# Performance work log

Hardware: AMD Instinct MI355X
Metric: run time of the kernel (lower is better)

The kernel has to match this reference:

```python
import jax, jax.numpy as jnp
import numpy as np

N = 10000      # nodes
E = 160000     # directed edges (avg degree 16)
F_IN = 2208    # num_features (DenseNet-161 dim)
H = 512        # hidden_channels
C = 2          # num_classes


def setup_inputs() -> dict:
    key = jax.random.key(0)
    ks = jax.random.split(key, 10)
    x = jax.random.normal(ks[0], (N, F_IN), dtype=jnp.float32)
    edge_index = jax.random.randint(ks[1], (2, E), 0, N, dtype=jnp.int64)
    batch = jnp.zeros((N,), dtype=jnp.int64)

    def glorot(k, fan_in, fan_out):
        s = np.sqrt(6.0 / (fan_in + fan_out)).astype(np.float32)
        return jax.random.uniform(k, (fan_in, fan_out), jnp.float32, -s, s)

    return {
        "x": x,
        "edge_index": edge_index,
        "batch": batch,
        "W1": glorot(ks[2], F_IN, H), "b1": jnp.zeros((H,), jnp.float32),
        "W2": glorot(ks[3], H, H),    "b2": jnp.zeros((H,), jnp.float32),
        "W3": glorot(ks[4], H, H),    "b3": jnp.zeros((H,), jnp.float32),
        "W4": glorot(ks[5], H, C),    "b4": jnp.zeros((C,), jnp.float32),
    }


def reference(x, edge_index, batch, W1, b1, W2, b2, W3, b3, W4, b4):
    # GCNConv (PyG defaults): add self-loops, symmetric normalization
    # out = D^{-1/2} (A + I) D^{-1/2} X W + b. Norm depends only on the
    # graph, so compute it once and reuse across the 4 layers.
    src, dst = edge_index[0], edge_index[1]
    loop = jnp.arange(N, dtype=edge_index.dtype)
    s = jnp.concatenate([src, loop])  # [E+N]
    d = jnp.concatenate([dst, loop])  # [E+N]
    deg = jax.ops.segment_sum(jnp.ones(E + N, x.dtype), d, num_segments=N)
    dinv = jnp.where(deg > 0, jax.lax.rsqrt(deg), 0.0)
    norm = dinv[s] * dinv[d]          # [E+N] per-edge weight

    def conv(h, W, b):
        h = h @ W                                 # [N, out] dense GEMM first (PyG order)
        msg = h[s] * norm[:, None]                # gather + scale  [E+N, out]
        return jax.ops.segment_sum(msg, d, num_segments=N) + b

    h = jax.nn.relu(conv(x, W1, b1))   # dropout p=0.3 is identity in eval mode
    h = jax.nn.relu(conv(h, W2, b2))
    h = jax.nn.relu(conv(h, W3, b3))
    h = conv(h, W4, b4)
    return jax.nn.log_softmax(h, axis=1)
```

## Files before the change

### kernel.cpp

```cpp
#include <hip/hip_runtime.h>
#include <hip/hip_bf16.h>

#define NNODES 10000
#define NEDGES 160000
#define FIN    2208
#define HDIM   512
#define NCLS   2

#define MPAD   10240
#define K1PAD  2240
#define BCAP   128

typedef __bf16 bf16x8 __attribute__((ext_vector_type(8)));
typedef float  f32x4  __attribute__((ext_vector_type(4)));
typedef unsigned short u16x8 __attribute__((ext_vector_type(8)));

__device__ inline unsigned short f2bf(float f) {
    union { float f; unsigned int u; } v; v.f = f;
    return (unsigned short)((v.u + 0x7FFFu + ((v.u >> 16) & 1u)) >> 16);
}
__device__ inline float bf2f(unsigned short u) {
    union { unsigned int i; float f; } v; v.i = ((unsigned int)u) << 16; return v.f;
}

__global__ void k_prep(const float* __restrict__ W1, const float* __restrict__ W2,
                       const float* __restrict__ W3, unsigned short* __restrict__ W1t,
                       unsigned short* __restrict__ W2t, unsigned short* __restrict__ W3t,
                       int* __restrict__ cnt) {
    int n = blockIdx.y;
    int bx = blockIdx.x;
    int t = threadIdx.x;
    if (bx < 9) {
        int k = bx * 256 + t;
        if (k < K1PAD) {
            float v = (k < FIN) ? W1[(size_t)k * HDIM + n] : 0.0f;
            W1t[(size_t)n * K1PAD + k] = f2bf(v);
        }
    } else if (bx < 11) {
        int k = (bx - 9) * 256 + t;
        W2t[(size_t)n * HDIM + k] = f2bf(W2[(size_t)k * HDIM + n]);
    } else if (bx < 13) {
        int k = (bx - 11) * 256 + t;
        W3t[(size_t)n * HDIM + k] = f2bf(W3[(size_t)k * HDIM + n]);
    } else {
        int i = n * 256 + t;
        if (i < NNODES) cnt[i] = 0;
    }
}

__global__ void k_cvt_fill(const float* __restrict__ x, unsigned short* __restrict__ xb,
                           const int* __restrict__ ei, int* __restrict__ cnt,
                           int* __restrict__ bucket) {
    int bx = blockIdx.x;
    int t = threadIdx.x;
    if (bx >= MPAD) {
        int i = (bx - MPAD) * 256 + t;
        if (i < NEDGES) {
            int src = ei[i];
            int dst = ei[NEDGES + i];
            int pos = atomicAdd(&cnt[dst], 1);
            bucket[dst * BCAP + pos] = src;
        }
        return;
    }
    int row = bx;
    unsigned short* orow = xb + (size_t)row * K1PAD;
    u16x8 z = {0, 0, 0, 0, 0, 0, 0, 0};
    if (row >= NNODES) {
        for (int c = t; c < K1PAD / 8; c += 256) *(u16x8*)(orow + c * 8) = z;
        return;
    }
    const float* irow = x + (size_t)row * FIN;
    for (int c = t; c < K1PAD / 8; c += 256) {
        int col = c * 8;
        u16x8 o = z;
        if (col + 8 <= FIN) {
            float4 f0 = *(const float4*)(irow + col);
            float4 f1 = *(const float4*)(irow + col + 4);
            o[0] = f2bf(f0.x); o[1] = f2bf(f0.y); o[2] = f2bf(f0.z); o[3] = f2bf(f0.w);
            o[4] = f2bf(f1.x); o[5] = f2bf(f1.y); o[6] = f2bf(f1.z); o[7] = f2bf(f1.w);
        }
        *(u16x8*)(orow + col) = o;
    }
}

#define BKK 64
#define GG1 640

__device__ __forceinline__ void gemm_body(
    const unsigned short* __restrict__ A, const unsigned short* __restrict__ Bt,
    unsigned short* __restrict__ C, int M, int K, int l) {
    __shared__ char As[128 * BKK * 2] __attribute__((aligned(16)));
    __shared__ char Bs[64 * BKK * 2]  __attribute__((aligned(16)));
    const int tid  = threadIdx.x;
    const int lane = tid & 63;
    const int w    = tid >> 6;
    const int wm   = w & 1, wn = w >> 1;
    const int quad = lane >> 4, lq = lane & 15;

    const int xcd   = l & 7;
    const int q     = l >> 3;
    const int strip = (q >> 3) * 8 + xcd;
    const int bm    = strip * 128;
    const int bn    = (q & 7) * 64;

    f32x4 acc[4][2] = {};

    for (int k0 = 0; k0 < K; k0 += BKK) {
        #pragma unroll
        for (int i = 0; i < 4; ++i) {
            int c = i * 256 + tid;
            int r = c >> 3;
            int g = (c & 7) ^ (r & 7);
            const char* gpA = (const char*)A + ((size_t)(bm + r) * K + k0) * 2 + (g << 4);
            __builtin_amdgcn_global_load_lds(
                (const __attribute__((address_space(1))) void*)gpA,
                (__attribute__((address_space(3))) void*)(As + c * 16), 16, 0, 0);
        }
        #pragma unroll
        for (int i = 0; i < 2; ++i) {
            int c = i * 256 + tid;
            int r = c >> 3;
            int g = (c & 7) ^ (r & 7);
            const char* gpB = (const char*)Bt + ((size_t)(bn + r) * K + k0) * 2 + (g << 4);
            __builtin_amdgcn_global_load_lds(
                (const __attribute__((address_space(1))) void*)gpB,
                (__attribute__((address_space(3))) void*)(Bs + c * 16), 16, 0, 0);
        }
        __syncthreads();

        #pragma unroll
        for (int s = 0; s < 2; ++s) {
            bf16x8 af[4], bfr[2];
            int g = s * 4 + quad;
            #pragma unroll
            for (int i = 0; i < 4; ++i) {
                int r = wm * 64 + i * 16 + lq;
                af[i] = *(const bf16x8*)(As + r * 128 + ((g ^ (r & 7)) << 4));
            }
            #pragma unroll
            for (int j = 0; j < 2; ++j) {
                int n = wn * 32 + j * 16 + lq;
                bfr[j] = *(const bf16x8*)(Bs + n * 128 + ((g ^ (n & 7)) << 4));
            }
            #pragma unroll
            for (int i = 0; i < 4; ++i)
                #pragma unroll
                for (int j = 0; j < 2; ++j)
                    acc[i][j] = __builtin_amdgcn_mfma_f32_16x16x32_bf16(
                        af[i], bfr[j], acc[i][j], 0, 0, 0);
        }
        __syncthreads();
    }

    #pragma unroll
    for (int i = 0; i < 4; ++i) {
        #pragma unroll
        for (int p = 0; p < 4; ++p) {
            int r = bm + wm * 64 + i * 16 + quad * 4 + p;
            if (r < M) {
                #pragma unroll
                for (int j = 0; j < 2; ++j) {
                    int col = bn + wn * 32 + j * 16 + lq;
                    C[(size_t)r * HDIM + col] = f2bf(acc[i][j][p]);
                }
            }
        }
    }
}

__global__ __launch_bounds__(256) void k_gemm1_dinv(
    const unsigned short* __restrict__ A, const unsigned short* __restrict__ Bt,
    unsigned short* __restrict__ C, int M, int K,
    const int* __restrict__ cnt, float* __restrict__ dinv) {
    int bx = blockIdx.x;
    if (bx < GG1) { gemm_body(A, Bt, C, M, K, bx); return; }
    int i = (bx - GG1) * 256 + threadIdx.x;
    if (i < NNODES) dinv[i] = rsqrtf((float)cnt[i] + 1.0f);
}

__global__ __launch_bounds__(256) void k_gemm_bf16(
    const unsigned short* __restrict__ A, const unsigned short* __restrict__ Bt,
    unsigned short* __restrict__ C, int M, int K) {
    gemm_body(A, Bt, C, M, K, blockIdx.x);
}


__global__ void k_agg(const unsigned short* __restrict__ Y, const float* __restrict__ dinv,
                      const int* __restrict__ cnt, const int* __restrict__ bucket,
                      const float* __restrict__ bias, unsigned short* __restrict__ Hb) {
    int w = (blockIdx.x * blockDim.x + threadIdx.x) >> 6;
    int lane = threadIdx.x & 63;
    if (w >= MPAD) return;
    unsigned short* hr = Hb + (size_t)w * HDIM + lane * 8;
    if (w >= NNODES) {
        u16x8 z = {0, 0, 0, 0, 0, 0, 0, 0};
        *(u16x8*)hr = z;
        return;
    }
    float di = dinv[w];
    float sw = di * di;
    u16x8 own = *(const u16x8*)(Y + (size_t)w * HDIM + lane * 8);
    float acc[8];
    #pragma unroll
    for (int t = 0; t < 8; ++t) acc[t] = sw * bf2f(own[t]);

    const int* col = bucket + w * BCAP;
    int deg = cnt[w];
    int e = 0;
    for (; e + 4 <= deg; e += 4) {
        int s0 = col[e + 0], s1 = col[e + 1];
        int s2 = col[e + 2], s3 = col[e + 3];
        float w0 = di * dinv[s0], w1 = di * dinv[s1];
        float w2 = di * dinv[s2], w3 = di * dinv[s3];
        u16x8 v0 = *(const u16x8*)(Y + (size_t)s0 * HDIM + lane * 8);
        u16x8 v1 = *(const u16x8*)(Y + (size_t)s1 * HDIM + lane * 8);
        u16x8 v2 = *(const u16x8*)(Y + (size_t)s2 * HDIM + lane * 8);
        u16x8 v3 = *(const u16x8*)(Y + (size_t)s3 * HDIM + lane * 8);
        #pragma unroll
        for (int t = 0; t < 8; ++t) {
            acc[t] += w0 * bf2f(v0[t]);
            acc[t] += w1 * bf2f(v1[t]);
            acc[t] += w2 * bf2f(v2[t]);
            acc[t] += w3 * bf2f(v3[t]);
        }
    }
    for (; e < deg; ++e) {
        int s = col[e];
        float wg = di * dinv[s];
        u16x8 v = *(const u16x8*)(Y + (size_t)s * HDIM + lane * 8);
        #pragma unroll
        for (int t = 0; t < 8; ++t) acc[t] += wg * bf2f(v[t]);
    }

    float4 b0 = ((const float4*)bias)[lane * 2];
    float4 b1 = ((const float4*)bias)[lane * 2 + 1];
    acc[0] += b0.x; acc[1] += b0.y; acc[2] += b0.z; acc[3] += b0.w;
    acc[4] += b1.x; acc[5] += b1.y; acc[6] += b1.z; acc[7] += b1.w;
    u16x8 o;
    #pragma unroll
    for (int t = 0; t < 8; ++t) o[t] = f2bf(fmaxf(acc[t], 0.0f));
    *(u16x8*)hr = o;
}


__global__ void k_agg_g4(const unsigned short* __restrict__ Y, const float* __restrict__ dinv,
                         const int* __restrict__ cnt, const int* __restrict__ bucket,
                         const float* __restrict__ b3, const float* __restrict__ W4,
                         float* __restrict__ Y4) {
    int w = (blockIdx.x * blockDim.x + threadIdx.x) >> 6;
    int lane = threadIdx.x & 63;
    if (w >= NNODES) return;
    float di = dinv[w];
    float sw = di * di;
    u16x8 own = *(const u16x8*)(Y + (size_t)w * HDIM + lane * 8);
    float acc[8];
    #pragma unroll
    for (int t = 0; t < 8; ++t) acc[t] = sw * bf2f(own[t]);

    const int* col = bucket + w * BCAP;
    int deg = cnt[w];
    int e = 0;
    for (; e + 4 <= deg; e += 4) {
        int s0 = col[e + 0], s1 = col[e + 1];
        int s2 = col[e + 2], s3 = col[e + 3];
        float w0 = di * dinv[s0], w1 = di * dinv[s1];
        float w2 = di * dinv[s2], w3 = di * dinv[s3];
        u16x8 v0 = *(const u16x8*)(Y + (size_t)s0 * HDIM + lane * 8);
        u16x8 v1 = *(const u16x8*)(Y + (size_t)s1 * HDIM + lane * 8);
        u16x8 v2 = *(const u16x8*)(Y + (size_t)s2 * HDIM + lane * 8);
        u16x8 v3 = *(const u16x8*)(Y + (size_t)s3 * HDIM + lane * 8);
        #pragma unroll
        for (int t = 0; t < 8; ++t) {
            acc[t] += w0 * bf2f(v0[t]);
            acc[t] += w1 * bf2f(v1[t]);
            acc[t] += w2 * bf2f(v2[t]);
            acc[t] += w3 * bf2f(v3[t]);
        }
    }
    for (; e < deg; ++e) {
        int s = col[e];
        float wg = di * dinv[s];
        u16x8 v = *(const u16x8*)(Y + (size_t)s * HDIM + lane * 8);
        #pragma unroll
        for (int t = 0; t < 8; ++t) acc[t] += wg * bf2f(v[t]);
    }

    float4 b0 = ((const float4*)b3)[lane * 2];
    float4 b1 = ((const float4*)b3)[lane * 2 + 1];
    acc[0] += b0.x; acc[1] += b0.y; acc[2] += b0.z; acc[3] += b0.w;
    acc[4] += b1.x; acc[5] += b1.y; acc[6] += b1.z; acc[7] += b1.w;
    #pragma unroll
    for (int t = 0; t < 8; ++t) acc[t] = fmaxf(acc[t], 0.0f);

    const float4* wf = (const float4*)W4;
    float4 w0 = wf[lane * 4 + 0];
    float4 w1 = wf[lane * 4 + 1];
    float4 w2 = wf[lane * 4 + 2];
    float4 w3 = wf[lane * 4 + 3];
    float z0 = acc[0]*w0.x + acc[1]*w0.z + acc[2]*w1.x + acc[3]*w1.z
             + acc[4]*w2.x + acc[5]*w2.z + acc[6]*w3.x + acc[7]*w3.z;
    float z1 = acc[0]*w0.y + acc[1]*w0.w + acc[2]*w1.y + acc[3]*w1.w
             + acc[4]*w2.y + acc[5]*w2.w + acc[6]*w3.y + acc[7]*w3.w;
    #pragma unroll
    for (int off = 32; off > 0; off >>= 1) {
        z0 += __shfl_down(z0, off);
        z1 += __shfl_down(z1, off);
    }
    if (lane == 0) {
        Y4[2 * w] = z0;
        Y4[2 * w + 1] = z1;
    }
}


__global__ void k_final(const float* __restrict__ Y4, const float* __restrict__ dinv,
                        const int* __restrict__ cnt, const int* __restrict__ bucket,
                        const float* __restrict__ b4, float* __restrict__ out, int n) {
    int i = blockIdx.x * blockDim.x + threadIdx.x;
    if (i >= n) return;
    float di = dinv[i];
    float sw = di * di;
    float z0 = sw * Y4[2 * i];
    float z1 = sw * Y4[2 * i + 1];
    const int* col = bucket + i * BCAP;
    int deg = cnt[i];
    for (int e = 0; e < deg; ++e) {
        int s = col[e];
        float wgt = di * dinv[s];
        z0 += wgt * Y4[2 * s];
        z1 += wgt * Y4[2 * s + 1];
    }
    z0 += b4[0];
    z1 += b4[1];
    float m = fmaxf(z0, z1);
    float l = m + logf(expf(z0 - m) + expf(z1 - m));
    out[2 * i] = z0 - l;
    out[2 * i + 1] = z1 - l;
}


extern "C" void kernel_launch(void* const* d_in, const int* in_sizes, int n_in,
                              void* d_out, int out_size, void* d_ws, size_t ws_size,
                              hipStream_t stream) {
    const float* x  = (const float*)d_in[0];
    const int*   ei = (const int*)d_in[1];
    const float* W1 = (const float*)d_in[3];
    const float* b1 = (const float*)d_in[4];
    const float* W2 = (const float*)d_in[5];
    const float* b2 = (const float*)d_in[6];
    const float* W3 = (const float*)d_in[7];
    const float* b3 = (const float*)d_in[8];
    const float* W4 = (const float*)d_in[9];
    const float* b4 = (const float*)d_in[10];
    float* out = (float*)d_out;

    char* ws = (char*)d_ws;
    float*          dinv    = (float*)(ws + 0);
    int*            cnt     = (int*)  (ws + 40960);
    int*            bucket  = (int*)  (ws + 81920);
    float*          Y4      = (float*)(ws + 5201920);
    unsigned short* xb      = (unsigned short*)(ws + 5283840);
    unsigned short* W1t     = (unsigned short*)(ws + 51159040);
    unsigned short* W2t     = (unsigned short*)(ws + 53452800);
    unsigned short* W3t     = (unsigned short*)(ws + 53977088);
    unsigned short* Yb      = (unsigned short*)(ws + 54501376);
    unsigned short* Hb      = (unsigned short*)(ws + 64987136);
    if (ws_size < 75472896) return;

    const int agrid = (MPAD * 64) / 256;

    k_prep<<<dim3(14, HDIM), 256, 0, stream>>>(W1, W2, W3, W1t, W2t, W3t, cnt);
    k_cvt_fill<<<MPAD + 625, 256, 0, stream>>>(x, xb, ei, cnt, bucket);
    k_gemm1_dinv<<<GG1 + 40, 256, 0, stream>>>(xb, W1t, Yb, NNODES, K1PAD, cnt, dinv);
    k_agg<<<agrid, 256, 0, stream>>>(Yb, dinv, cnt, bucket, b1, Hb);
    k_gemm_bf16<<<GG1, 256, 0, stream>>>(Hb, W2t, Yb, NNODES, HDIM);
    k_agg<<<agrid, 256, 0, stream>>>(Yb, dinv, cnt, bucket, b2, Hb);
    k_gemm_bf16<<<GG1, 256, 0, stream>>>(Hb, W3t, Yb, NNODES, HDIM);
    k_agg_g4<<<(NNODES * 64) / 256, 256, 0, stream>>>(Yb, dinv, cnt, bucket, b3, W4, Y4);
    k_final<<<40, 256, 0, stream>>>(Y4, dinv, cnt, bucket, b4, out, NNODES);
}
```

Before: 310.5 us.

## Enlarge GEMM tile to 128x128 and fuse weight prep with x conversion

The GEMM block tile grows from 128x64 to 128x128, so each wave computes a 64x64 sub-tile with 16 accumulators and the grid drops from 640 to 320 blocks. This raises reuse of the A tile and halves A reloads from global memory. Separately, weight transpose, x conversion and edge bucketing are merged into one launch, with a small zeroing kernel placed before it. The trade-offs are higher register and LDS use per block and fewer blocks (320) spread over the CUs, which could hurt occupancy.

Result: slower. 323.8 us (+4.3%).

```diff
diff --git a/kernel.cpp b/kernel.cpp
--- a/kernel.cpp
+++ b/kernel.cpp
@@ -23,75 +23,78 @@
     union { unsigned int i; float f; } v; v.i = ((unsigned int)u) << 16; return v.f;
 }
 
-__global__ void k_prep(const float* __restrict__ W1, const float* __restrict__ W2,
-                       const float* __restrict__ W3, unsigned short* __restrict__ W1t,
-                       unsigned short* __restrict__ W2t, unsigned short* __restrict__ W3t,
-                       int* __restrict__ cnt) {
-    int n = blockIdx.y;
-    int bx = blockIdx.x;
+__global__ void k_zero(int* __restrict__ cnt) {
+    int i = blockIdx.x * 256 + threadIdx.x;
+    if (i < NNODES) cnt[i] = 0;
+}
+
+#define PREPB 7168
+#define CVTB  10240
+__global__ void k_prep_cvt_fill(
+    const float* __restrict__ W1, const float* __restrict__ W2,
+    const float* __restrict__ W3, unsigned short* __restrict__ W1t,
+    unsigned short* __restrict__ W2t, unsigned short* __restrict__ W3t,
+    const float* __restrict__ x, unsigned short* __restrict__ xb,
+    const int* __restrict__ ei, int* __restrict__ cnt, int* __restrict__ bucket) {
+    int b = blockIdx.x;
     int t = threadIdx.x;
-    if (bx < 9) {
-        int k = bx * 256 + t;
-        if (k < K1PAD) {
-            float v = (k < FIN) ? W1[(size_t)k * HDIM + n] : 0.0f;
-            W1t[(size_t)n * K1PAD + k] = f2bf(v);
-        }
-    } else if (bx < 11) {
-        int k = (bx - 9) * 256 + t;
-        W2t[(size_t)n * HDIM + k] = f2bf(W2[(size_t)k * HDIM + n]);
-    } else if (bx < 13) {
-        int k = (bx - 11) * 256 + t;
-        W3t[(size_t)n * HDIM + k] = f2bf(W3[(size_t)k * HDIM + n]);
-    } else {
-        int i = n * 256 + t;
-        if (i < NNODES) cnt[i] = 0;
-    }
-}
-
-__global__ void k_cvt_fill(const float* __restrict__ x, unsigned short* __restrict__ xb,
-                           const int* __restrict__ ei, int* __restrict__ cnt,
-                           int* __restrict__ bucket) {
-    int bx = blockIdx.x;
-    int t = threadIdx.x;
-    if (bx >= MPAD) {
-        int i = (bx - MPAD) * 256 + t;
-        if (i < NEDGES) {
-            int src = ei[i];
-            int dst = ei[NEDGES + i];
-            int pos = atomicAdd(&cnt[dst], 1);
-            bucket[dst * BCAP + pos] = src;
+    if (b < PREPB) {
+        int bx = b % 14;
+        int n  = b / 14;
+        if (bx < 9) {
+            int k = bx * 256 + t;
+            if (k < K1PAD) {
+                float v = (k < FIN) ? W1[(size_t)k * HDIM + n] : 0.0f;
+                W1t[(size_t)n * K1PAD + k] = f2bf(v);
+            }
+        } else if (bx < 11) {
+            int k = (bx - 9) * 256 + t;
+            W2t[(size_t)n * HDIM + k] = f2bf(W2[(size_t)k * HDIM + n]);
+        } else if (bx < 13) {
+            int k = (bx - 11) * 256 + t;
+            W3t[(size_t)n * HDIM + k] = f2bf(W3[(size_t)k * HDIM + n]);
         }
         return;
     }
-    int row = bx;
-    unsigned short* orow = xb + (size_t)row * K1PAD;
-    u16x8 z = {0, 0, 0, 0, 0, 0, 0, 0};
-    if (row >= NNODES) {
-        for (int c = t; c < K1PAD / 8; c += 256) *(u16x8*)(orow + c * 8) = z;
+    if (b < PREPB + CVTB) {
+        int row = b - PREPB;
+        unsigned short* orow = xb + (size_t)row * K1PAD;
+        u16x8 z = {0, 0, 0, 0, 0, 0, 0, 0};
+        if (row >= NNODES) {
+            for (int c = t; c < K1PAD / 8; c += 256) *(u16x8*)(orow + c * 8) = z;
+            return;
+        }
+        const float* irow = x + (size_t)row * FIN;
+        for (int c = t; c < K1PAD / 8; c += 256) {
+            int col = c * 8;
+            u16x8 o = z;
+            if (col + 8 <= FIN) {
+                float4 f0 = *(const float4*)(irow + col);
+                float4 f1 = *(const float4*)(irow + col + 4);
+                o[0] = f2bf(f0.x); o[1] = f2bf(f0.y); o[2] = f2bf(f0.z); o[3] = f2bf(f0.w);
+                o[4] = f2bf(f1.x); o[5] = f2bf(f1.y); o[6] = f2bf(f1.z); o[7] = f2bf(f1.w);
+            }
+            *(u16x8*)(orow + col) = o;
+        }
         return;
     }
-    const float* irow = x + (size_t)row * FIN;
-    for (int c = t; c < K1PAD / 8; c += 256) {
-        int col = c * 8;
-        u16x8 o = z;
-        if (col + 8 <= FIN) {
-            float4 f0 = *(const float4*)(irow + col);
-            float4 f1 = *(const float4*)(irow + col + 4);
-            o[0] = f2bf(f0.x); o[1] = f2bf(f0.y); o[2] = f2bf(f0.z); o[3] = f2bf(f0.w);
-            o[4] = f2bf(f1.x); o[5] = f2bf(f1.y); o[6] = f2bf(f1.z); o[7] = f2bf(f1.w);
-        }
-        *(u16x8*)(orow + col) = o;
+    int i = (b - PREPB - CVTB) * 256 + t;
+    if (i < NEDGES) {
+        int src = ei[i];
+        int dst = ei[NEDGES + i];
+        int pos = atomicAdd(&cnt[dst], 1);
+        bucket[dst * BCAP + pos] = src;
     }
 }
 
 #define BKK 64
-#define GG1 640
+#define GB1 320
 
 __device__ __forceinline__ void gemm_body(
     const unsigned short* __restrict__ A, const unsigned short* __restrict__ Bt,
     unsigned short* __restrict__ C, int M, int K, int l) {
     __shared__ char As[128 * BKK * 2] __attribute__((aligned(16)));
-    __shared__ char Bs[64 * BKK * 2]  __attribute__((aligned(16)));
+    __shared__ char Bs[128 * BKK * 2] __attribute__((aligned(16)));
     const int tid  = threadIdx.x;
     const int lane = tid & 63;
     const int w    = tid >> 6;
@@ -100,11 +103,11 @@
 
     const int xcd   = l & 7;
     const int q     = l >> 3;
-    const int strip = (q >> 3) * 8 + xcd;
+    const int bn    = (q & 3) * 128;
+    const int strip = (q >> 2) * 8 + xcd;
     const int bm    = strip * 128;
-    const int bn    = (q & 7) * 64;
-
-    f32x4 acc[4][2] = {};
+
+    f32x4 acc[4][4] = {};
 
     for (int k0 = 0; k0 < K; k0 += BKK) {
         #pragma unroll
@@ -118,7 +121,7 @@
                 (__attribute__((address_space(3))) void*)(As + c * 16), 16, 0, 0);
         }
         #pragma unroll
-        for (int i = 0; i < 2; ++i) {
+        for (int i = 0; i < 4; ++i) {
             int c = i * 256 + tid;
             int r = c >> 3;
             int g = (c & 7) ^ (r & 7);
@@ -131,7 +134,7 @@
 
         #pragma unroll
         for (int s = 0; s < 2; ++s) {
-            bf16x8 af[4], bfr[2];
+            bf16x8 af[4], bfr[4];
             int g = s * 4 + quad;
             #pragma unroll
             for (int i = 0; i < 4; ++i) {
@@ -139,14 +142,14 @@
                 af[i] = *(const bf16x8*)(As + r * 128 + ((g ^ (r & 7)) << 4));
             }
             #pragma unroll
-            for (int j = 0; j < 2; ++j) {
-                int n = wn * 32 + j * 16 + lq;
+            for (int j = 0; j < 4; ++j) {
+                int n = wn * 64 + j * 16 + lq;
                 bfr[j] = *(const bf16x8*)(Bs + n * 128 + ((g ^ (n & 7)) << 4));
             }
             #pragma unroll
             for (int i = 0; i < 4; ++i)
                 #pragma unroll
-                for (int j = 0; j < 2; ++j)
+                for (int j = 0; j < 4; ++j)
                     acc[i][j] = __builtin_amdgcn_mfma_f32_16x16x32_bf16(
                         af[i], bfr[j], acc[i][j], 0, 0, 0);
         }
@@ -160,8 +163,8 @@
             int r = bm + wm * 64 + i * 16 + quad * 4 + p;
             if (r < M) {
                 #pragma unroll
-                for (int j = 0; j < 2; ++j) {
-                    int col = bn + wn * 32 + j * 16 + lq;
+                for (int j = 0; j < 4; ++j) {
+                    int col = bn + wn * 64 + j * 16 + lq;
                     C[(size_t)r * HDIM + col] = f2bf(acc[i][j][p]);
                 }
             }
@@ -174,8 +177,8 @@
     unsigned short* __restrict__ C, int M, int K,
     const int* __restrict__ cnt, float* __restrict__ dinv) {
     int bx = blockIdx.x;
-    if (bx < GG1) { gemm_body(A, Bt, C, M, K, bx); return; }
-    int i = (bx - GG1) * 256 + threadIdx.x;
+    if (bx < GB1) { gemm_body(A, Bt, C, M, K, bx); return; }
+    int i = (bx - GB1) * 256 + threadIdx.x;
     if (i < NNODES) dinv[i] = rsqrtf((float)cnt[i] + 1.0f);
 }
 
@@ -184,7 +187,6 @@
     unsigned short* __restrict__ C, int M, int K) {
     gemm_body(A, Bt, C, M, K, blockIdx.x);
 }
-
 
 __global__ void k_agg(const unsigned short* __restrict__ Y, const float* __restrict__ dinv,
                       const int* __restrict__ cnt, const int* __restrict__ bucket,
@@ -243,7 +245,6 @@
     *(u16x8*)hr = o;
 }
 
-
 __global__ void k_agg_g4(const unsigned short* __restrict__ Y, const float* __restrict__ dinv,
                          const int* __restrict__ cnt, const int* __restrict__ bucket,
                          const float* __restrict__ b3, const float* __restrict__ W4,
@@ -312,7 +313,6 @@
         Y4[2 * w + 1] = z1;
     }
 }
-
 
 __global__ void k_final(const float* __restrict__ Y4, const float* __restrict__ dinv,
                         const int* __restrict__ cnt, const int* __restrict__ bucket,
@@ -370,13 +370,14 @@
 
     const int agrid = (MPAD * 64) / 256;
 
-    k_prep<<<dim3(14, HDIM), 256, 0, stream>>>(W1, W2, W3, W1t, W2t, W3t, cnt);
-    k_cvt_fill<<<MPAD + 625, 256, 0, stream>>>(x, xb, ei, cnt, bucket);
-    k_gemm1_dinv<<<GG1 + 40, 256, 0, stream>>>(xb, W1t, Yb, NNODES, K1PAD, cnt, dinv);
+    k_zero<<<40, 256, 0, stream>>>(cnt);
+    k_prep_cvt_fill<<<PREPB + CVTB + 625, 256, 0, stream>>>(
+        W1, W2, W3, W1t, W2t, W3t, x, xb, ei, cnt, bucket);
+    k_gemm1_dinv<<<GB1 + 40, 256, 0, stream>>>(xb, W1t, Yb, NNODES, K1PAD, cnt, dinv);
     k_agg<<<agrid, 256, 0, stream>>>(Yb, dinv, cnt, bucket, b1, Hb);
-    k_gemm_bf16<<<GG1, 256, 0, stream>>>(Hb, W2t, Yb, NNODES, HDIM);
+    k_gemm_bf16<<<GB1, 256, 0, stream>>>(Hb, W2t, Yb, NNODES, HDIM);
     k_agg<<<agrid, 256, 0, stream>>>(Yb, dinv, cnt, bucket, b2, Hb);
-    k_gemm_bf16<<<GG1, 256, 0, stream>>>(Hb, W3t, Yb, NNODES, HDIM);
+    k_gemm_bf16<<<GB1, 256, 0, stream>>>(Hb, W3t, Yb, NNODES, HDIM);
     k_agg_g4<<<(NNODES * 64) / 256, 256, 0, stream>>>(Yb, dinv, cnt, bucket, b3, W4, Y4);
     k_final<<<40, 256, 0, stream>>>(Y4, dinv, cnt, bucket, b4, out, NNODES);
 }
```
